# Kernel optimization log

Measured on AMD Instinct MI355X. Metric: run time of the kernel, lower is better.

## Reference

```python
import jax, jax.numpy as jnp
import numpy as np

C = 1024
HEAD = 128

def setup_inputs() -> dict:
    key = jax.random.key(0)
    kx, kq, kk, kv = jax.random.split(key, 4)
    x = jax.random.normal(kx, (8, 2048, C), dtype=jnp.float32)
    s = 1.0 / np.sqrt(C)
    Wq = jax.random.normal(kq, (C, HEAD), dtype=jnp.float32) * s
    Wk = jax.random.normal(kk, (C, HEAD), dtype=jnp.float32) * s
    Wv = jax.random.normal(kv, (C, HEAD), dtype=jnp.float32) * s
    return {"x": x, "Wq": Wq, "Wk": Wk, "Wv": Wv}

def reference(x, Wq, Wk, Wv):
    B, T, Cdim = x.shape
    q = jnp.einsum('btc,ch->bth', x, Wq)
    k = jnp.einsum('btc,ch->bth', x, Wk)
    v = jnp.einsum('btc,ch->bth', x, Wv)
    # scores scaled by C**-0.5 (faithful to source, which uses input width C)
    wei = jnp.einsum('bqh,bkh->bqk', q, k) * (Cdim ** -0.5)
    causal = jnp.tril(jnp.ones((T, T), dtype=bool))
    wei = jnp.where(causal, wei, -jnp.inf)
    wei = jax.nn.softmax(wei, axis=-1)
    # dropout p=0.0 -> identity
    return jnp.einsum('bqk,bkh->bqh', wei, v)
```

## Files before the change

### kernel.cpp

```cpp
#include <hip/hip_runtime.h>
#include <hip/hip_bf16.h>


typedef __attribute__((ext_vector_type(8))) short bf16x8;
typedef __attribute__((ext_vector_type(4))) short short4v;
typedef __attribute__((ext_vector_type(4))) float f32x4;

#define NB   8
#define TT   2048
#define CDIM 1024
#define HD   128
#define NTOK (NB * TT)
#define NW   384

using bf16 = __hip_bfloat16;

__device__ __forceinline__ short f2bs(float f) {
    unsigned u = __builtin_bit_cast(unsigned, f);
    return (short)((u + 0x7FFF + ((u >> 16) & 1)) >> 16);
}

__global__ __launch_bounds__(256) void prep_w_kernel(
        const float* __restrict__ Wq, const float* __restrict__ Wk,
        const float* __restrict__ Wv, bf16* __restrict__ Wp) {
    const int f  = blockIdx.x * 256 + threadIdx.x;
    const int l  = f & 63;
    const int nt = (f >> 6) % 24;
    const int sl = f / 1536;
    const int ln = l & 15, quad = l >> 4;
    const int n  = nt * 16 + ln;
    const int w  = n >> 7, h = n & 127;
    const float* W = (w == 0) ? Wq : (w == 1) ? Wk : Wv;
    const int k0 = sl * 32 + quad * 8;
    bf16x8 frag;
    #pragma unroll
    for (int j = 0; j < 8; j++)
        frag[j] = f2bs(W[(long)(k0 + j) * HD + h]);
    *(bf16x8*)((short*)Wp + (long)f * 8) = frag;
}

__global__ __launch_bounds__(512, 4) void qkv_proj_kernel(
        const float* __restrict__ x, const bf16* __restrict__ Wp,
        bf16* __restrict__ Q, bf16* __restrict__ Kp, bf16* __restrict__ Vp) {
    __shared__ __align__(16) char smem[32768];
    const int tid  = threadIdx.x;
    const int wave = tid >> 6, lane = tid & 63;
    const int quad = lane >> 4, ln = lane & 15;
    const long mbase = (long)blockIdx.x * 32;

    const float* srow[4];
    int woffs[4];
    #pragma unroll
    for (int j = 0; j < 4; j++) {
        const int row = j * 8 + wave;
        srow[j]  = x + (mbase + row) * CDIM + lane * 4;
        woffs[j] = row * 512 + ((lane * 8) ^ ((row & 7) << 4));
    }
    const int xorv = (ln & 7) << 4;

    const f32x4 zero = {0.f, 0.f, 0.f, 0.f};
    f32x4 acc[2][3];
    #pragma unroll
    for (int mt = 0; mt < 2; mt++)
        #pragma unroll
        for (int nt = 0; nt < 3; nt++) acc[mt][nt] = zero;

    const short* bps = (const short*)Wp + (long)wave * 1536 + lane * 8;

    #pragma unroll
    for (int j = 0; j < 4; j++) {
        float4 v = *(const float4*)(srow[j]);
        short4v s4 = { f2bs(v.x), f2bs(v.y), f2bs(v.z), f2bs(v.w) };
        *(short4v*)(smem + woffs[j]) = s4;
    }
    __syncthreads();

    for (int g = 0; g < 4; ++g) {
        float4 xn[4];
        if (g < 3) {
            #pragma unroll
            for (int j = 0; j < 4; j++)
                xn[j] = *(const float4*)(srow[j] + (g + 1) * 256);
        }
        const char* bb = smem + (g & 1) * 16384;
        #pragma unroll
        for (int s = 0; s < 8; ++s) {
            const int sg = g * 8 + s;
            bf16x8 b0 = *(const bf16x8*)(bps + (long)sg * 12288);
            bf16x8 b1 = *(const bf16x8*)(bps + (long)sg * 12288 + 512);
            bf16x8 b2 = *(const bf16x8*)(bps + (long)sg * 12288 + 1024);
            const int cb = (s * 64 + quad * 16) ^ xorv;
            bf16x8 af0 = *(const bf16x8*)(bb + ln * 512 + cb);
            bf16x8 af1 = *(const bf16x8*)(bb + (16 + ln) * 512 + cb);
            acc[0][0] = __builtin_amdgcn_mfma_f32_16x16x32_bf16(af0, b0, acc[0][0], 0, 0, 0);
            acc[0][1] = __builtin_amdgcn_mfma_f32_16x16x32_bf16(af0, b1, acc[0][1], 0, 0, 0);
            acc[0][2] = __builtin_amdgcn_mfma_f32_16x16x32_bf16(af0, b2, acc[0][2], 0, 0, 0);
            acc[1][0] = __builtin_amdgcn_mfma_f32_16x16x32_bf16(af1, b0, acc[1][0], 0, 0, 0);
            acc[1][1] = __builtin_amdgcn_mfma_f32_16x16x32_bf16(af1, b1, acc[1][1], 0, 0, 0);
            acc[1][2] = __builtin_amdgcn_mfma_f32_16x16x32_bf16(af1, b2, acc[1][2], 0, 0, 0);
        }
        if (g < 3) {
            char* bn = smem + ((g + 1) & 1) * 16384;
            #pragma unroll
            for (int j = 0; j < 4; j++) {
                short4v s4 = { f2bs(xn[j].x), f2bs(xn[j].y),
                               f2bs(xn[j].z), f2bs(xn[j].w) };
                *(short4v*)(bn + woffs[j]) = s4;
            }
        }
        __syncthreads();
    }

    short* kT = (short*)smem;
    short* vT = (short*)smem + 8192;
    #pragma unroll
    for (int mt = 0; mt < 2; mt++) {
        #pragma unroll
        for (int nt = 0; nt < 3; nt++) {
            const int n = wave * 48 + nt * 16 + ln;
            #pragma unroll
            for (int r = 0; r < 4; r++) {
                const int row = mt * 16 + quad * 4 + r;
                const short hv = f2bs(acc[mt][nt][r]);
                if (n < 128) {
                    long gg = mbase + row;
                    int b = (int)(gg >> 11), t = (int)(gg & (TT - 1));
                    Q[((long)b * TT + t) * HD + n] = __builtin_bit_cast(bf16, hv);
                } else if (n < 256) {
                    kT[row * 136 + (n - 128)] = hv;
                } else {
                    vT[(n - 256) * 40 + row] = hv;
                }
            }
        }
    }
    __syncthreads();

    {
        const long tile = blockIdx.x;
        const int  kc = wave >> 1, ntk = wave & 1;
        bf16x8 kv = *(const bf16x8*)&kT[(ntk*16 + ln)*136 + kc*32 + quad*8];
        *(bf16x8*)((short*)Kp + (tile*8 + wave)*512 + lane*8) = kv;
        bf16x8 vv = *(const bf16x8*)&vT[(wave*16 + ln)*40 + quad*8];
        *(bf16x8*)((short*)Vp + (tile*8 + wave)*512 + lane*8) = vv;
    }
}

__global__ __launch_bounds__(256, 2) void attn_kernel(
        const bf16* __restrict__ Q, const bf16* __restrict__ Kp,
        const bf16* __restrict__ Vp, float* __restrict__ out) {
    __shared__ __align__(16) char smem[33024];

    const int tid  = threadIdx.x;
    const int wave = tid >> 6, lane = tid & 63;
    const int quad = lane >> 4, ln = lane & 15;
    const int b   = blockIdx.x & 7;
    const int idx = blockIdx.x >> 3;
    const int qi  = (idx >> 5) ? (idx & 31) : 63 - (idx & 31);
    const int qb  = qi * 32;
    const int ntiles = qi + 1;
    const int t0 = (ntiles * wave) >> 2;
    const int t1 = (ntiles * (wave + 1)) >> 2;

    const bf16*  Qb  = Q + (long)b * TT * HD;
    const short* Kpb = (const short*)Kp + (long)b * 64 * 4096;
    const short* Vpb = (const short*)Vp + (long)b * 64 * 4096;

    short* pwave = (short*)smem + wave * 2560;

    bf16x8 qf[2][4];
    #pragma unroll
    for (int mt = 0; mt < 2; mt++)
        #pragma unroll
        for (int kc = 0; kc < 4; kc++)
            qf[mt][kc] = *(const bf16x8*)(Qb + (long)(qb + mt*16 + ln)*HD + kc*32 + quad*8);

    const f32x4 zero = {0.f, 0.f, 0.f, 0.f};
    f32x4 o[2][8];
    #pragma unroll
    for (int mt = 0; mt < 2; mt++)
        #pragma unroll
        for (int ht = 0; ht < 8; ht++) o[mt][ht] = zero;
    float li[2][4] = {{0.f,0.f,0.f,0.f},{0.f,0.f,0.f,0.f}};

    for (int kt = t0; kt < t1; ++kt) {
        const int j0 = kt * 32;
        const short* kbase = Kpb + (long)kt * 4096 + lane * 8;
        bf16x8 kf[4][2];
        #pragma unroll
        for (int kc = 0; kc < 4; kc++)
            #pragma unroll
            for (int nt = 0; nt < 2; nt++)
                kf[kc][nt] = *(const bf16x8*)(kbase + (kc*2 + nt)*512);

        f32x4 s[2][2];
        s[0][0] = zero; s[0][1] = zero; s[1][0] = zero; s[1][1] = zero;
        #pragma unroll
        for (int kc = 0; kc < 4; kc++)
            #pragma unroll
            for (int mt = 0; mt < 2; mt++) {
                s[mt][0] = __builtin_amdgcn_mfma_f32_16x16x32_bf16(qf[mt][kc], kf[kc][0], s[mt][0], 0, 0, 0);
                s[mt][1] = __builtin_amdgcn_mfma_f32_16x16x32_bf16(qf[mt][kc], kf[kc][1], s[mt][1], 0, 0, 0);
            }

        short* pb = pwave + (kt & 1) * 1280;
        #pragma unroll
        for (int mt = 0; mt < 2; mt++)
            #pragma unroll
            for (int r = 0; r < 4; r++) {
                const int q = qb + mt*16 + quad*4 + r;
                #pragma unroll
                for (int nt = 0; nt < 2; nt++) {
                    float p = __expf(s[mt][nt][r] * 0.03125f);
                    if (j0 + nt*16 + ln > q) p = 0.f;
                    li[mt][r] += p;
                    pb[(mt*16 + quad*4 + r)*40 + nt*16 + ln] = f2bs(p);
                }
            }

        const short* vbase = Vpb + (long)kt * 4096 + lane * 8;
        bf16x8 vf[8];
        #pragma unroll
        for (int ht = 0; ht < 8; ht++)
            vf[ht] = *(const bf16x8*)(vbase + ht*512);

        bf16x8 pf[2];
        #pragma unroll
        for (int mt = 0; mt < 2; mt++)
            pf[mt] = *(const bf16x8*)&pb[(mt*16 + ln)*40 + quad*8];
        #pragma unroll
        for (int mt = 0; mt < 2; mt++)
            #pragma unroll
            for (int ht = 0; ht < 8; ht++)
                o[mt][ht] = __builtin_amdgcn_mfma_f32_16x16x32_bf16(pf[mt], vf[ht], o[mt][ht], 0, 0, 0);
    }

    #pragma unroll
    for (int mt = 0; mt < 2; mt++)
        #pragma unroll
        for (int r = 0; r < 4; r++)
            #pragma unroll
            for (int d = 1; d < 16; d <<= 1) li[mt][r] += __shfl_xor(li[mt][r], d);

    __syncthreads();
    float* red  = (float*)smem;
    float* redl = (float*)(smem + 32768);
    if (wave & 1) {
        const int slot = wave >> 1;
        #pragma unroll
        for (int mt = 0; mt < 2; mt++)
            #pragma unroll
            for (int ht = 0; ht < 8; ht++)
                #pragma unroll
                for (int r = 0; r < 4; r++)
                    red[slot*4096 + (mt*16 + quad*4 + r)*128 + ht*16 + ln] = o[mt][ht][r];
        if (ln == 0)
            #pragma unroll
            for (int mt = 0; mt < 2; mt++)
                #pragma unroll
                for (int r = 0; r < 4; r++)
                    redl[slot*32 + mt*16 + quad*4 + r] = li[mt][r];
    }
    __syncthreads();
    if (!(wave & 1)) {
        const int slot = wave >> 1;
        #pragma unroll
        for (int mt = 0; mt < 2; mt++) {
            #pragma unroll
            for (int ht = 0; ht < 8; ht++)
                #pragma unroll
                for (int r = 0; r < 4; r++)
                    o[mt][ht][r] += red[slot*4096 + (mt*16 + quad*4 + r)*128 + ht*16 + ln];
            #pragma unroll
            for (int r = 0; r < 4; r++)
                li[mt][r] += redl[slot*32 + mt*16 + quad*4 + r];
        }
    }
    __syncthreads();
    if (wave == 2) {
        #pragma unroll
        for (int mt = 0; mt < 2; mt++) {
            #pragma unroll
            for (int ht = 0; ht < 8; ht++)
                #pragma unroll
                for (int r = 0; r < 4; r++)
                    red[(mt*16 + quad*4 + r)*128 + ht*16 + ln] = o[mt][ht][r];
            if (ln == 0)
                #pragma unroll
                for (int r = 0; r < 4; r++)
                    redl[mt*16 + quad*4 + r] = li[mt][r];
        }
    }
    __syncthreads();
    if (wave == 0) {
        #pragma unroll
        for (int mt = 0; mt < 2; mt++) {
            #pragma unroll
            for (int r = 0; r < 4; r++)
                li[mt][r] += redl[mt*16 + quad*4 + r];
            #pragma unroll
            for (int ht = 0; ht < 8; ht++)
                #pragma unroll
                for (int r = 0; r < 4; r++) {
                    float v = o[mt][ht][r] + red[(mt*16 + quad*4 + r)*128 + ht*16 + ln];
                    out[((long)b*TT + qb + mt*16 + quad*4 + r)*HD + ht*16 + ln] = v / li[mt][r];
                }
        }
    }
}

extern "C" void kernel_launch(void* const* d_in, const int* in_sizes, int n_in,
                              void* d_out, int out_size, void* d_ws, size_t ws_size,
                              hipStream_t stream) {
    const float* x  = (const float*)d_in[0];
    const float* Wq = (const float*)d_in[1];
    const float* Wk = (const float*)d_in[2];
    const float* Wv = (const float*)d_in[3];
    float* outp = (float*)d_out;

    bf16* Wp = (bf16*)d_ws;
    bf16* Qm = Wp + (long)NW * CDIM;
    bf16* Kp = Qm + (long)NTOK * HD;
    bf16* Vp = Kp + (long)NTOK * HD;

    prep_w_kernel<<<192, 256, 0, stream>>>(Wq, Wk, Wv, Wp);
    qkv_proj_kernel<<<512, 512, 0, stream>>>(x, Wp, Qm, Kp, Vp);
    attn_kernel<<<NB * 64, 256, 0, stream>>>(Qm, Kp, Vp, outp);
}
```

Baseline: 148.3 us.

## Split attention block into 8 waves by query half and key segment

The attention kernel moves from 256 to 512 threads per block. Each wave now handles a single 16-row query half over one quarter of the key tiles, instead of both halves. This halves the accumulator registers per wave and doubles the waves available to hide latency. In exchange, K and V fragments are loaded twice per block. The cross-wave reduction becomes a single shared-memory pass into the segment-0 waves, using more shared memory.

```diff
diff --git a/kernel.cpp b/kernel.cpp
--- a/kernel.cpp
+++ b/kernel.cpp
@@ -146,42 +146,40 @@
     }
 }
 
-__global__ __launch_bounds__(256, 2) void attn_kernel(
+__global__ __launch_bounds__(512, 2) void attn_kernel(
         const bf16* __restrict__ Q, const bf16* __restrict__ Kp,
         const bf16* __restrict__ Vp, float* __restrict__ out) {
-    __shared__ __align__(16) char smem[33024];
+    __shared__ __align__(16) char smem[49536];
 
     const int tid  = threadIdx.x;
     const int wave = tid >> 6, lane = tid & 63;
     const int quad = lane >> 4, ln = lane & 15;
+    const int mt   = wave & 1, seg = wave >> 1;
+
     const int b   = blockIdx.x & 7;
     const int idx = blockIdx.x >> 3;
     const int qi  = (idx >> 5) ? (idx & 31) : 63 - (idx & 31);
-    const int qb  = qi * 32;
-    const int ntiles = qi + 1;
-    const int t0 = (ntiles * wave) >> 2;
-    const int t1 = (ntiles * (wave + 1)) >> 2;
+    const int qb  = qi * 32 + mt * 16;
+    const int nt  = qi + 1;
+    const int t0  = (nt * seg) >> 2;
+    const int t1  = (nt * (seg + 1)) >> 2;
 
     const bf16*  Qb  = Q + (long)b * TT * HD;
     const short* Kpb = (const short*)Kp + (long)b * 64 * 4096;
     const short* Vpb = (const short*)Vp + (long)b * 64 * 4096;
 
-    short* pwave = (short*)smem + wave * 2560;
-
-    bf16x8 qf[2][4];
-    #pragma unroll
-    for (int mt = 0; mt < 2; mt++)
-        #pragma unroll
-        for (int kc = 0; kc < 4; kc++)
-            qf[mt][kc] = *(const bf16x8*)(Qb + (long)(qb + mt*16 + ln)*HD + kc*32 + quad*8);
+    short* pwave = (short*)smem + wave * 1280;
+
+    bf16x8 qf[4];
+    #pragma unroll
+    for (int kc = 0; kc < 4; kc++)
+        qf[kc] = *(const bf16x8*)(Qb + (long)(qb + ln)*HD + kc*32 + quad*8);
 
     const f32x4 zero = {0.f, 0.f, 0.f, 0.f};
-    f32x4 o[2][8];
-    #pragma unroll
-    for (int mt = 0; mt < 2; mt++)
-        #pragma unroll
-        for (int ht = 0; ht < 8; ht++) o[mt][ht] = zero;
-    float li[2][4] = {{0.f,0.f,0.f,0.f},{0.f,0.f,0.f,0.f}};
+    f32x4 o[8];
+    #pragma unroll
+    for (int ht = 0; ht < 8; ht++) o[ht] = zero;
+    float li[4] = {0.f, 0.f, 0.f, 0.f};
 
     for (int kt = t0; kt < t1; ++kt) {
         const int j0 = kt * 32;
@@ -190,33 +188,28 @@
         #pragma unroll
         for (int kc = 0; kc < 4; kc++)
             #pragma unroll
-            for (int nt = 0; nt < 2; nt++)
-                kf[kc][nt] = *(const bf16x8*)(kbase + (kc*2 + nt)*512);
-
-        f32x4 s[2][2];
-        s[0][0] = zero; s[0][1] = zero; s[1][0] = zero; s[1][1] = zero;
-        #pragma unroll
-        for (int kc = 0; kc < 4; kc++)
-            #pragma unroll
-            for (int mt = 0; mt < 2; mt++) {
-                s[mt][0] = __builtin_amdgcn_mfma_f32_16x16x32_bf16(qf[mt][kc], kf[kc][0], s[mt][0], 0, 0, 0);
-                s[mt][1] = __builtin_amdgcn_mfma_f32_16x16x32_bf16(qf[mt][kc], kf[kc][1], s[mt][1], 0, 0, 0);
+            for (int ntk = 0; ntk < 2; ntk++)
+                kf[kc][ntk] = *(const bf16x8*)(kbase + (kc*2 + ntk)*512);
+
+        f32x4 s[2]; s[0] = zero; s[1] = zero;
+        #pragma unroll
+        for (int kc = 0; kc < 4; kc++) {
+            s[0] = __builtin_amdgcn_mfma_f32_16x16x32_bf16(qf[kc], kf[kc][0], s[0], 0, 0, 0);
+            s[1] = __builtin_amdgcn_mfma_f32_16x16x32_bf16(qf[kc], kf[kc][1], s[1], 0, 0, 0);
+        }
+
+        short* pb = pwave + (kt & 1) * 640;
+        #pragma unroll
+        for (int r = 0; r < 4; r++) {
+            const int q = qb + quad*4 + r;
+            #pragma unroll
+            for (int ntk = 0; ntk < 2; ntk++) {
+                float p = __expf(s[ntk][r] * 0.03125f);
+                if (j0 + ntk*16 + ln > q) p = 0.f;
+                li[r] += p;
+                pb[(quad*4 + r)*40 + ntk*16 + ln] = f2bs(p);
             }
-
-        short* pb = pwave + (kt & 1) * 1280;
-        #pragma unroll
-        for (int mt = 0; mt < 2; mt++)
-            #pragma unroll
-            for (int r = 0; r < 4; r++) {
-                const int q = qb + mt*16 + quad*4 + r;
-                #pragma unroll
-                for (int nt = 0; nt < 2; nt++) {
-                    float p = __expf(s[mt][nt][r] * 0.03125f);
-                    if (j0 + nt*16 + ln > q) p = 0.f;
-                    li[mt][r] += p;
-                    pb[(mt*16 + quad*4 + r)*40 + nt*16 + ln] = f2bs(p);
-                }
-            }
+        }
 
         const short* vbase = Vpb + (long)kt * 4096 + lane * 8;
         bf16x8 vf[8];
@@ -224,88 +217,51 @@
         for (int ht = 0; ht < 8; ht++)
             vf[ht] = *(const bf16x8*)(vbase + ht*512);
 
-        bf16x8 pf[2];
-        #pragma unroll
-        for (int mt = 0; mt < 2; mt++)
-            pf[mt] = *(const bf16x8*)&pb[(mt*16 + ln)*40 + quad*8];
-        #pragma unroll
-        for (int mt = 0; mt < 2; mt++)
-            #pragma unroll
-            for (int ht = 0; ht < 8; ht++)
-                o[mt][ht] = __builtin_amdgcn_mfma_f32_16x16x32_bf16(pf[mt], vf[ht], o[mt][ht], 0, 0, 0);
-    }
-
-    #pragma unroll
-    for (int mt = 0; mt < 2; mt++)
-        #pragma unroll
-        for (int r = 0; r < 4; r++)
-            #pragma unroll
-            for (int d = 1; d < 16; d <<= 1) li[mt][r] += __shfl_xor(li[mt][r], d);
+        bf16x8 pf = *(const bf16x8*)&pb[ln*40 + quad*8];
+        #pragma unroll
+        for (int ht = 0; ht < 8; ht++)
+            o[ht] = __builtin_amdgcn_mfma_f32_16x16x32_bf16(pf, vf[ht], o[ht], 0, 0, 0);
+    }
+
+    #pragma unroll
+    for (int r = 0; r < 4; r++)
+        #pragma unroll
+        for (int d = 1; d < 16; d <<= 1) li[r] += __shfl_xor(li[r], d);
 
     __syncthreads();
     float* red  = (float*)smem;
-    float* redl = (float*)(smem + 32768);
-    if (wave & 1) {
-        const int slot = wave >> 1;
-        #pragma unroll
-        for (int mt = 0; mt < 2; mt++)
+    float* redl = (float*)(smem + 49152);
+    if (seg > 0) {
+        const int slot = mt * 3 + (seg - 1);
+        #pragma unroll
+        for (int ht = 0; ht < 8; ht++)
+            #pragma unroll
+            for (int r = 0; r < 4; r++)
+                red[slot*2048 + (quad*4 + r)*128 + ht*16 + ln] = o[ht][r];
+        if (ln == 0)
+            #pragma unroll
+            for (int r = 0; r < 4; r++)
+                redl[slot*16 + quad*4 + r] = li[r];
+    }
+    __syncthreads();
+    if (seg == 0) {
+        #pragma unroll
+        for (int s = 0; s < 3; s++) {
+            const int slot = mt * 3 + s;
             #pragma unroll
             for (int ht = 0; ht < 8; ht++)
                 #pragma unroll
                 for (int r = 0; r < 4; r++)
-                    red[slot*4096 + (mt*16 + quad*4 + r)*128 + ht*16 + ln] = o[mt][ht][r];
-        if (ln == 0)
-            #pragma unroll
-            for (int mt = 0; mt < 2; mt++)
-                #pragma unroll
-                for (int r = 0; r < 4; r++)
-                    redl[slot*32 + mt*16 + quad*4 + r] = li[mt][r];
-    }
-    __syncthreads();
-    if (!(wave & 1)) {
-        const int slot = wave >> 1;
-        #pragma unroll
-        for (int mt = 0; mt < 2; mt++) {
-            #pragma unroll
-            for (int ht = 0; ht < 8; ht++)
-                #pragma unroll
-                for (int r = 0; r < 4; r++)
-                    o[mt][ht][r] += red[slot*4096 + (mt*16 + quad*4 + r)*128 + ht*16 + ln];
-            #pragma unroll
-            for (int r = 0; r < 4; r++)
-                li[mt][r] += redl[slot*32 + mt*16 + quad*4 + r];
-        }
-    }
-    __syncthreads();
-    if (wave == 2) {
-        #pragma unroll
-        for (int mt = 0; mt < 2; mt++) {
-            #pragma unroll
-            for (int ht = 0; ht < 8; ht++)
-                #pragma unroll
-                for (int r = 0; r < 4; r++)
-                    red[(mt*16 + quad*4 + r)*128 + ht*16 + ln] = o[mt][ht][r];
-            if (ln == 0)
-                #pragma unroll
-                for (int r = 0; r < 4; r++)
-                    redl[mt*16 + quad*4 + r] = li[mt][r];
-        }
-    }
-    __syncthreads();
-    if (wave == 0) {
-        #pragma unroll
-        for (int mt = 0; mt < 2; mt++) {
-            #pragma unroll
-            for (int r = 0; r < 4; r++)
-                li[mt][r] += redl[mt*16 + quad*4 + r];
-            #pragma unroll
-            for (int ht = 0; ht < 8; ht++)
-                #pragma unroll
-                for (int r = 0; r < 4; r++) {
-                    float v = o[mt][ht][r] + red[(mt*16 + quad*4 + r)*128 + ht*16 + ln];
-                    out[((long)b*TT + qb + mt*16 + quad*4 + r)*HD + ht*16 + ln] = v / li[mt][r];
-                }
-        }
+                    o[ht][r] += red[slot*2048 + (quad*4 + r)*128 + ht*16 + ln];
+            #pragma unroll
+            for (int r = 0; r < 4; r++)
+                li[r] += redl[slot*16 + quad*4 + r];
+        }
+        #pragma unroll
+        for (int ht = 0; ht < 8; ht++)
+            #pragma unroll
+            for (int r = 0; r < 4; r++)
+                out[((long)b*TT + qb + quad*4 + r)*HD + ht*16 + ln] = o[ht][r] / li[r];
     }
 }
 
@@ -325,5 +281,5 @@
 
     prep_w_kernel<<<192, 256, 0, stream>>>(Wq, Wk, Wv, Wp);
     qkv_proj_kernel<<<512, 512, 0, stream>>>(x, Wp, Qm, Kp, Vp);
-    attn_kernel<<<NB * 64, 256, 0, stream>>>(Qm, Kp, Vp, outp);
-}
+    attn_kernel<<<NB * 64, 512, 0, stream>>>(Qm, Kp, Vp, outp);
+}
```

New measurement: 154.2 us. +4.0%, slower.
